# Kernel optimization log

Hardware: AMD Instinct MI355X
Metric: run time of the kernel (lower is better)

Reference implementation:

```python
import jax, jax.numpy as jnp
import numpy as np

N, L, E, H = 4, 2048, 1024, 16
D = E // H  # head_dim = 64


def setup_inputs() -> dict:
    key = jax.random.key(0)
    ks = jax.random.split(key, 9)
    return {
        "values": jax.random.normal(ks[0], (N, L, E), jnp.float32),
        "keys": jax.random.normal(ks[1], (N, L, E), jnp.float32),
        "queries": jax.random.normal(ks[2], (N, L, E), jnp.float32),
        "mask": jax.random.randint(ks[3], (N, 1, L, L), 0, 2, jnp.int32),
        "Wq": jax.random.normal(ks[4], (D, D), jnp.float32) * (1.0 / np.sqrt(D)),
        "Wk": jax.random.normal(ks[5], (D, D), jnp.float32) * (1.0 / np.sqrt(D)),
        "Wv": jax.random.normal(ks[6], (D, D), jnp.float32) * (1.0 / np.sqrt(D)),
        "Wo": jax.random.normal(ks[7], (E, E), jnp.float32) * (1.0 / np.sqrt(E)),
        "bo": jax.random.normal(ks[8], (E,), jnp.float32) * 0.01,
    }


def reference(values, keys, queries, mask, Wq, Wk, Wv, Wo, bo):
    n, ql, _ = queries.shape
    kl = keys.shape[1]
    # split heads: [N, L, H, D]
    q = queries.reshape(n, ql, H, D)
    k = keys.reshape(n, kl, H, D)
    v = values.reshape(n, kl, H, D)
    # per-head linear projections (torch Linear: x @ W.T), shared across heads
    q = jnp.einsum('nqhd,ed->nqhe', q, Wq)
    k = jnp.einsum('nkhd,ed->nkhe', k, Wk)
    v = jnp.einsum('nkhd,ed->nkhe', v, Wv)
    # scores [N, H, Q, K]
    energy = jnp.einsum('nqhd,nkhd->nhqk', q, k)
    energy = jnp.where(mask == 0, jnp.float32(-1e20), energy)
    attn = jax.nn.softmax(energy / jnp.sqrt(jnp.float32(E)), axis=3)
    out = jnp.einsum('nhqk,nkhd->nqhd', attn, v).reshape(n, ql, E)
    return out @ Wo.T + bo
```

## Files before the change

kernel.cpp:

```cpp
#include <hip/hip_runtime.h>
#include <stdint.h>


static constexpr int N_ = 4, L_ = 2048, E_ = 1024, H_ = 16, D_ = 64;

typedef __bf16 bf16_t;
typedef __attribute__((ext_vector_type(8))) __bf16 bf16x8;
typedef __attribute__((ext_vector_type(4))) float f32x4;
typedef __attribute__((ext_vector_type(16))) float f32x16;
typedef __attribute__((ext_vector_type(4))) unsigned int uint4v;
typedef __attribute__((ext_vector_type(2))) unsigned int uint2v;

__device__ __forceinline__ f32x16 mfma32(bf16x8 a, bf16x8 b, f32x16 c) {
    return __builtin_amdgcn_mfma_f32_32x32x16_bf16(a, b, c, 0, 0, 0);
}
__device__ __forceinline__ unsigned int pk2(float a, float b) {
    union { bf16_t h[2]; unsigned int u; } z;
    z.h[0] = (bf16_t)a; z.h[1] = (bf16_t)b;
    return z.u;
}
#define GLOAD16(g, l)                                                        \
    __builtin_amdgcn_global_load_lds(                                        \
        (const __attribute__((address_space(1))) void*)(g),                  \
        (__attribute__((address_space(3))) void*)(l), 16, 0, 0)

__global__ __launch_bounds__(256) void pack_mask_k(
    const int* __restrict__ mask, unsigned int* __restrict__ mpkT) {
    int wid  = blockIdx.x * 4 + (threadIdx.x >> 6);
    int lane = threadIdx.x & 63;
    int c = wid & 31;
    int q = (wid >> 5) & (L_ - 1);
    int n = wid >> 16;
    int v = mask[((size_t)n * L_ + q) * L_ + c * 64 + lane];
    unsigned long long b = __ballot(v != 0);
    if (lane == 0) {
        mpkT[((size_t)n * 64 + 2 * c) * L_ + q]     = (unsigned int)b;
        mpkT[((size_t)n * 64 + 2 * c + 1) * L_ + q] = (unsigned int)(b >> 32);
    }
}

__global__ __launch_bounds__(256) void cvt_wo_k(
    const float* __restrict__ Wo, bf16_t* __restrict__ WoB) {
    int i = blockIdx.x * 256 + threadIdx.x;
    WoB[i] = (bf16_t)Wo[i];
}

__global__ __launch_bounds__(256) void proj_mfma_k(
    const float* __restrict__ qin, const float* __restrict__ kin,
    const float* __restrict__ vin,
    const float* __restrict__ Wq, const float* __restrict__ Wk,
    const float* __restrict__ Wv,
    bf16_t* __restrict__ qB, bf16_t* __restrict__ kB, bf16_t* __restrict__ vT) {
    int which = blockIdx.z;
    int h = blockIdx.y;
    const float* in = (which == 0) ? qin : (which == 1) ? kin : vin;
    const float* W  = (which == 0) ? Wq  : (which == 1) ? Wk  : Wv;
    int w = threadIdx.x >> 6, lane = threadIdx.x & 63;
    int lo5 = lane & 31, hi = lane >> 5;
    int rbase = blockIdx.x * 128 + w * 32;
    int n = rbase >> 11;
    int lloc = rbase & (L_ - 1);
    int nh = n * H_ + h;

    bf16x8 xf[4];
    const float* xrow = in + (size_t)(rbase + lo5) * E_ + h * 64 + hi * 8;
    #pragma unroll
    for (int c = 0; c < 4; ++c) {
        float4 f0 = *(const float4*)(xrow + c * 16);
        float4 f1 = *(const float4*)(xrow + c * 16 + 4);
        bf16x8 v;
        v[0] = (bf16_t)f0.x; v[1] = (bf16_t)f0.y; v[2] = (bf16_t)f0.z; v[3] = (bf16_t)f0.w;
        v[4] = (bf16_t)f1.x; v[5] = (bf16_t)f1.y; v[6] = (bf16_t)f1.z; v[7] = (bf16_t)f1.w;
        xf[c] = v;
    }
    bf16x8 wf[2][4];
    #pragma unroll
    for (int t2 = 0; t2 < 2; ++t2) {
        const float* wrow = W + (size_t)(t2 * 32 + lo5) * 64 + hi * 8;
        #pragma unroll
        for (int c = 0; c < 4; ++c) {
            float4 f0 = *(const float4*)(wrow + c * 16);
            float4 f1 = *(const float4*)(wrow + c * 16 + 4);
            bf16x8 v;
            v[0] = (bf16_t)f0.x; v[1] = (bf16_t)f0.y; v[2] = (bf16_t)f0.z; v[3] = (bf16_t)f0.w;
            v[4] = (bf16_t)f1.x; v[5] = (bf16_t)f1.y; v[6] = (bf16_t)f1.z; v[7] = (bf16_t)f1.w;
            wf[t2][c] = v;
        }
    }
    f32x16 acc0, acc1;
    #pragma unroll
    for (int r = 0; r < 16; ++r) { acc0[r] = 0.f; acc1[r] = 0.f; }

    if (which != 2) {
        #pragma unroll
        for (int c = 0; c < 4; ++c) {
            acc0 = mfma32(xf[c], wf[0][c], acc0);
            acc1 = mfma32(xf[c], wf[1][c], acc1);
        }
        const float osc = (which == 0) ? (0.03125f * 1.44269504f) : 1.0f;
        bf16_t* outp = ((which == 0) ? qB : kB) + ((size_t)nh * L_ + lloc) * 64;
        #pragma unroll
        for (int r = 0; r < 16; ++r) {
            int qr = (r & 3) + 8 * (r >> 2) + 4 * hi;
            outp[qr * 64 + lo5]      = (bf16_t)(acc0[r] * osc);
            outp[qr * 64 + 32 + lo5] = (bf16_t)(acc1[r] * osc);
        }
    } else {
        #pragma unroll
        for (int c = 0; c < 4; ++c) {
            acc0 = mfma32(wf[0][c], xf[c], acc0);
            acc1 = mfma32(wf[1][c], xf[c], acc1);
        }
        bf16_t* outp = vT + (size_t)nh * 64 * L_ + lloc;
        #pragma unroll
        for (int r = 0; r < 16; ++r) {
            int dr = (r & 3) + 8 * (r >> 2) + 4 * hi;
            outp[(size_t)dr * L_ + lo5]        = (bf16_t)acc0[r];
            outp[(size_t)(dr + 32) * L_ + lo5] = (bf16_t)acc1[r];
        }
    }
}

__global__ __launch_bounds__(512) void attn_lds_k(
    const bf16_t* __restrict__ qB, const bf16_t* __restrict__ kB,
    const bf16_t* __restrict__ vT, const unsigned int* __restrict__ mpkT,
    bf16_t* __restrict__ aoB) {
    __shared__ alignas(16) unsigned char smem[16384];
    int b = blockIdx.x;
    int xcd = b & 7, idx = b >> 3;
    int nh = xcd * 8 + (idx >> 3);
    int qt = idx & 7;
    int n = nh >> 4, h = nh & 15;
    int tid = threadIdx.x;
    int w = tid >> 6, lane = tid & 63;
    int lo5 = lane & 31, hi = lane >> 5;
    int q0 = qt * 256 + w * 32;

    const bf16_t* qb = qB + ((size_t)nh * L_ + q0) * D_;
    const bf16_t* kblk = kB + (size_t)nh * L_ * D_;
    const bf16_t* vblk = vT + (size_t)nh * D_ * L_;
    const unsigned int* mptr = mpkT + (size_t)n * 64 * L_ + q0 + lo5;

    unsigned char* my_lds_base = smem + (size_t)(tid >> 6) * 1024;
    size_t g_off;
    if (tid < 256) {
        int r = tid >> 3, c = tid & 7;
        g_off = (size_t)r * 64 + ((c ^ (r & 7)) * 8);
    } else {
        int v = tid - 256;
        int d = v >> 2, j = v & 3;
        g_off = (size_t)d * L_ + ((j ^ ((d >> 1) & 3)) * 8);
    }
    const size_t gstep = (tid < 256) ? (size_t)(32 * 64) : (size_t)32;
    const bf16_t* gnext = ((tid < 256) ? kblk : vblk) + g_off;

    bf16x8 qf[4];
    #pragma unroll
    for (int c = 0; c < 4; ++c)
        qf[c] = *(const bf16x8*)(qb + lo5 * D_ + c * 16 + hi * 8);

    f32x16 o0, o1;
    #pragma unroll
    for (int r = 0; r < 16; ++r) { o0[r] = 0.f; o1[r] = 0.f; }
    float lsum = 0.f;
    int vsw = (lo5 >> 1) & 3;

    f32x16 kZero;
    #pragma unroll
    for (int r = 0; r < 16; ++r) kZero[r] = 0.f;

    GLOAD16(gnext, my_lds_base);  gnext += gstep;
    unsigned int mw = *mptr; mptr += L_;

    #pragma unroll 1
    for (int t = 0; t < 64; ++t) {
        int cur = t & 1;
        unsigned int mw_n = *mptr; mptr += L_;
        if (t < 63) {
            GLOAD16(gnext, my_lds_base + (cur ^ 1) * 8192);
            gnext += gstep;
            asm volatile("s_waitcnt vmcnt(1)" ::: "memory");
        } else {
            asm volatile("s_waitcnt vmcnt(0)" ::: "memory");
        }
        __builtin_amdgcn_s_barrier();
        __builtin_amdgcn_sched_barrier(0);

        const bf16_t* Kb = (const bf16_t*)(smem + cur * 8192);
        const bf16_t* Vb = Kb + 2048;
        __builtin_amdgcn_s_setprio(1);
        bf16x8 kf0 = *(const bf16x8*)(Kb + lo5 * 64 + ((hi ^ (lo5 & 7)) << 3));
        f32x16 st = mfma32(kf0, qf[0], kZero);
        #pragma unroll
        for (int c = 1; c < 4; ++c) {
            bf16x8 kfc = *(const bf16x8*)(Kb + lo5 * 64 +
                                          ((((c << 1) | hi) ^ (lo5 & 7)) << 3));
            st = mfma32(kfc, qf[c], st);
        }
        __builtin_amdgcn_s_setprio(0);
        const bf16_t* vrow0 = Vb + lo5 * 32;
        const bf16_t* vrow1 = Vb + (lo5 + 32) * 32;
        bf16x8 v00 = *(const bf16x8*)(vrow0 + ((hi ^ vsw) << 3));
        bf16x8 v01 = *(const bf16x8*)(vrow0 + (((2 | hi) ^ vsw) << 3));
        bf16x8 v10 = *(const bf16x8*)(vrow1 + ((hi ^ vsw) << 3));
        bf16x8 v11 = *(const bf16x8*)(vrow1 + (((2 | hi) ^ vsw) << 3));
        float p[16];
        #pragma unroll
        for (int r = 0; r < 16; ++r) p[r] = exp2f(st[r]);
        unsigned int mws = hi ? (mw >> 4) : mw;
        #pragma unroll
        for (int r = 0; r < 16; ++r) {
            int kr = (r & 3) + 8 * (r >> 2);
            int mm = __builtin_amdgcn_sbfe(mws, kr, 1);
            p[r] = __uint_as_float(__float_as_uint(p[r]) & (unsigned int)mm);
        }
        float s0 = (p[0] + p[1]) + (p[2] + p[3]);
        float s1 = (p[4] + p[5]) + (p[6] + p[7]);
        float s2 = (p[8] + p[9]) + (p[10] + p[11]);
        float s3 = (p[12] + p[13]) + (p[14] + p[15]);
        lsum += (s0 + s1) + (s2 + s3);
        unsigned int w0 = pk2(p[0],  p[1]),  w1 = pk2(p[2],  p[3]);
        unsigned int w2 = pk2(p[4],  p[5]),  w3 = pk2(p[6],  p[7]);
        unsigned int w4 = pk2(p[8],  p[9]),  w5 = pk2(p[10], p[11]);
        unsigned int w6 = pk2(p[12], p[13]), w7 = pk2(p[14], p[15]);
        uint2v s02 = __builtin_amdgcn_permlane32_swap(w0, w2, false, false);
        uint2v s13 = __builtin_amdgcn_permlane32_swap(w1, w3, false, false);
        uint2v s46 = __builtin_amdgcn_permlane32_swap(w4, w6, false, false);
        uint2v s57 = __builtin_amdgcn_permlane32_swap(w5, w7, false, false);
        uint4v fa0, fa1;
        fa0.x = s02.x; fa0.y = s13.x; fa0.z = s02.y; fa0.w = s13.y;
        fa1.x = s46.x; fa1.y = s57.x; fa1.z = s46.y; fa1.w = s57.y;
        bf16x8 pa0 = __builtin_bit_cast(bf16x8, fa0);
        bf16x8 pa1 = __builtin_bit_cast(bf16x8, fa1);
        __builtin_amdgcn_s_setprio(1);
        o0 = mfma32(pa0, v00, o0);
        o1 = mfma32(pa0, v10, o1);
        o0 = mfma32(pa1, v01, o0);
        o1 = mfma32(pa1, v11, o1);
        __builtin_amdgcn_s_setprio(0);
        mw = mw_n;
        __builtin_amdgcn_s_barrier();
        __builtin_amdgcn_sched_barrier(0);
    }

    float lt = lsum + __shfl_xor(lsum, 32);
    #pragma unroll
    for (int r = 0; r < 16; ++r) {
        int qr = (r & 3) + 8 * (r >> 2) + 4 * hi;
        float inv = __builtin_amdgcn_rcpf(__shfl(lt, qr));
        bf16_t* orow = aoB + ((size_t)n * L_ + q0 + qr) * E_ + h * 64;
        orow[lo5]      = (bf16_t)(o0[r] * inv);
        orow[32 + lo5] = (bf16_t)(o1[r] * inv);
    }
}

__global__ __launch_bounds__(256) void out_gemm_lds_k(
    const bf16_t* __restrict__ A, const bf16_t* __restrict__ WoB,
    const float* __restrict__ bo, float* __restrict__ Y) {
    __shared__ alignas(16) unsigned char bsm[32768];
    int b = blockIdx.x;
    int ct = b & 7, rt = b >> 3;
    int tid = threadIdx.x;
    int w = tid >> 6, lane = tid & 63;
    int lo5 = lane & 31, hi = lane >> 5;
    int row0 = rt * 128, col0 = ct * 128;
    const bf16_t* arow = A + (size_t)(row0 + w * 32 + lo5) * E_ + hi * 8;

    f32x16 acc0, acc1, acc2, acc3;
    #pragma unroll
    for (int r = 0; r < 16; ++r) { acc0[r]=0.f; acc1[r]=0.f; acc2[r]=0.f; acc3[r]=0.f; }

    auto stageB = [&](int kc, int buf) {
        #pragma unroll
        for (int rr = 0; rr < 4; ++rr) {
            int g = tid + rr * 256;
            int nn = g >> 3, slot = g & 7;
            const bf16_t* src = WoB + (size_t)(col0 + nn) * E_ + kc * 64 +
                                ((slot ^ (nn & 7)) * 8);
            GLOAD16(src, bsm + (size_t)buf * 16384 + (size_t)(w * 64 + rr * 256) * 16);
        }
    };

    stageB(0, 0);
    #pragma unroll 1
    for (int kc = 0; kc < 16; ++kc) {
        int cur = kc & 1;
        if (kc < 15) stageB(kc + 1, cur ^ 1);
        if (kc < 15) { asm volatile("s_waitcnt vmcnt(4)" ::: "memory"); }
        else         { asm volatile("s_waitcnt vmcnt(0)" ::: "memory"); }
        __builtin_amdgcn_s_barrier();
        __builtin_amdgcn_sched_barrier(0);
        const bf16_t* Bl = (const bf16_t*)(bsm + (size_t)cur * 16384);
        #pragma unroll
        for (int c = 0; c < 4; ++c) {
            bf16x8 af = *(const bf16x8*)(arow + kc * 64 + c * 16);
            int slot = ((((c << 1) | hi) ^ (lo5 & 7)) << 3);
            bf16x8 b0 = *(const bf16x8*)(Bl + (0 * 32 + lo5) * 64 + slot);
            bf16x8 b1 = *(const bf16x8*)(Bl + (1 * 32 + lo5) * 64 + slot);
            bf16x8 b2 = *(const bf16x8*)(Bl + (2 * 32 + lo5) * 64 + slot);
            bf16x8 b3 = *(const bf16x8*)(Bl + (3 * 32 + lo5) * 64 + slot);
            __builtin_amdgcn_s_setprio(1);
            acc0 = mfma32(af, b0, acc0);
            acc1 = mfma32(af, b1, acc1);
            acc2 = mfma32(af, b2, acc2);
            acc3 = mfma32(af, b3, acc3);
            __builtin_amdgcn_s_setprio(0);
        }
        __builtin_amdgcn_s_barrier();
        __builtin_amdgcn_sched_barrier(0);
    }

    #define EPI(ACC, CG)                                                     \
    {                                                                        \
        float bias = bo[col0 + (CG) * 32 + lo5];                             \
        _Pragma("unroll")                                                    \
        for (int r = 0; r < 16; ++r) {                                       \
            int qr = (r & 3) + 8 * (r >> 2) + 4 * hi;                        \
            Y[(size_t)(row0 + w * 32 + qr) * E_ + col0 + (CG) * 32 + lo5] =  \
                ACC[r] + bias;                                               \
        }                                                                    \
    }
    EPI(acc0, 0) EPI(acc1, 1) EPI(acc2, 2) EPI(acc3, 3)
    #undef EPI
}

extern "C" void kernel_launch(void* const* d_in, const int* in_sizes, int n_in,
                              void* d_out, int out_size, void* d_ws, size_t ws_size,
                              hipStream_t stream) {
    const float* values  = (const float*)d_in[0];
    const float* keys    = (const float*)d_in[1];
    const float* queries = (const float*)d_in[2];
    const int*   mask    = (const int*)  d_in[3];
    const float* Wq      = (const float*)d_in[4];
    const float* Wk      = (const float*)d_in[5];
    const float* Wv      = (const float*)d_in[6];
    const float* Wo      = (const float*)d_in[7];
    const float* bo      = (const float*)d_in[8];
    float* Y = (float*)d_out;

    const size_t SZ = (size_t)N_ * H_ * L_ * D_;
    bf16_t* qB  = (bf16_t*)d_ws;
    bf16_t* kB  = qB + SZ;
    bf16_t* vT  = kB + SZ;
    bf16_t* aoB = vT + SZ;
    unsigned int* mpkT = (unsigned int*)(aoB + SZ);
    bf16_t* WoB = (bf16_t*)(mpkT + (size_t)N_ * 64 * L_);

    pack_mask_k<<<N_ * L_ * 32 / 4, 256, 0, stream>>>(mask, mpkT);
    cvt_wo_k<<<E_ * E_ / 256, 256, 0, stream>>>(Wo, WoB);
    proj_mfma_k<<<dim3(N_ * L_ / 128, H_, 3), 256, 0, stream>>>(
        queries, keys, values, Wq, Wk, Wv, qB, kB, vT);
    attn_lds_k<<<N_ * H_ * (L_ / 256), 512, 0, stream>>>(
        qB, kB, vT, mpkT, aoB);
    out_gemm_lds_k<<<(E_ / 128) * (N_ * L_ / 128), 256, 0, stream>>>(
        aoB, WoB, bo, Y);
}
```

Before: 240.7 us.

## Halve attention block size and unroll double-buffered K/V loop by two

The attention kernel now launches 256-thread blocks covering 128 queries instead of 512-thread blocks covering 256. Twice as many blocks are launched, and each thread loads both K and V tiles instead of splitting the loads across thread halves. The main loop is unrolled by two with fixed buffer pointers, LDS offsets are precomputed, and it uses the raw exp2 builtin and packed float2 sums. The goal is more blocks per CU, less address arithmetic and lighter barriers. The cost is that each block re-reads the full K/V stream, so global and L2 traffic for K/V doubles.

```diff
diff --git a/kernel.cpp b/kernel.cpp
--- a/kernel.cpp
+++ b/kernel.cpp
@@ -6,6 +6,7 @@
 
 typedef __bf16 bf16_t;
 typedef __attribute__((ext_vector_type(8))) __bf16 bf16x8;
+typedef __attribute__((ext_vector_type(2))) float f32x2;
 typedef __attribute__((ext_vector_type(4))) float f32x4;
 typedef __attribute__((ext_vector_type(16))) float f32x16;
 typedef __attribute__((ext_vector_type(4))) unsigned int uint4v;
@@ -121,104 +122,92 @@
     }
 }
 
-__global__ __launch_bounds__(512) void attn_lds_k(
+__global__ __launch_bounds__(256) void attn_lds_k(
     const bf16_t* __restrict__ qB, const bf16_t* __restrict__ kB,
     const bf16_t* __restrict__ vT, const unsigned int* __restrict__ mpkT,
     bf16_t* __restrict__ aoB) {
     __shared__ alignas(16) unsigned char smem[16384];
     int b = blockIdx.x;
     int xcd = b & 7, idx = b >> 3;
-    int nh = xcd * 8 + (idx >> 3);
-    int qt = idx & 7;
+    int nh = xcd * 8 + (idx >> 4);
+    int qt = idx & 15;
     int n = nh >> 4, h = nh & 15;
     int tid = threadIdx.x;
     int w = tid >> 6, lane = tid & 63;
     int lo5 = lane & 31, hi = lane >> 5;
-    int q0 = qt * 256 + w * 32;
+    int q0 = qt * 128 + w * 32;
 
     const bf16_t* qb = qB + ((size_t)nh * L_ + q0) * D_;
     const bf16_t* kblk = kB + (size_t)nh * L_ * D_;
     const bf16_t* vblk = vT + (size_t)nh * D_ * L_;
     const unsigned int* mptr = mpkT + (size_t)n * 64 * L_ + q0 + lo5;
 
-    unsigned char* my_lds_base = smem + (size_t)(tid >> 6) * 1024;
-    size_t g_off;
-    if (tid < 256) {
-        int r = tid >> 3, c = tid & 7;
-        g_off = (size_t)r * 64 + ((c ^ (r & 7)) * 8);
-    } else {
-        int v = tid - 256;
-        int d = v >> 2, j = v & 3;
-        g_off = (size_t)d * L_ + ((j ^ ((d >> 1) & 3)) * 8);
-    }
-    const size_t gstep = (tid < 256) ? (size_t)(32 * 64) : (size_t)32;
-    const bf16_t* gnext = ((tid < 256) ? kblk : vblk) + g_off;
+    int kr_ = tid >> 3, kc_ = tid & 7;
+    int vd_ = tid >> 2, vj_ = tid & 3;
+    const bf16_t* gK = kblk + kr_ * 64 + ((kc_ ^ (kr_ & 7)) * 8);
+    const bf16_t* gV = vblk + (size_t)vd_ * L_ + ((vj_ ^ ((vd_ >> 1) & 3)) * 8);
+    unsigned ldsK = (unsigned)(w * 1024);
+    unsigned ldsV = (unsigned)(4096 + w * 1024);
 
     bf16x8 qf[4];
     #pragma unroll
     for (int c = 0; c < 4; ++c)
         qf[c] = *(const bf16x8*)(qb + lo5 * D_ + c * 16 + hi * 8);
 
+    int koff0 = lo5 * 64 + (((0 | hi) ^ (lo5 & 7)) << 3);
+    int koff1 = lo5 * 64 + (((2 | hi) ^ (lo5 & 7)) << 3);
+    int koff2 = lo5 * 64 + (((4 | hi) ^ (lo5 & 7)) << 3);
+    int koff3 = lo5 * 64 + (((6 | hi) ^ (lo5 & 7)) << 3);
+    int vsw = (lo5 >> 1) & 3;
+    int voff0a = lo5 * 32 + ((hi ^ vsw) << 3);
+    int voff0b = lo5 * 32 + (((2 | hi) ^ vsw) << 3);
+    int voff1a = (lo5 + 32) * 32 + ((hi ^ vsw) << 3);
+    int voff1b = (lo5 + 32) * 32 + (((2 | hi) ^ vsw) << 3);
+    int shv = hi << 2;
+
     f32x16 o0, o1;
     #pragma unroll
     for (int r = 0; r < 16; ++r) { o0[r] = 0.f; o1[r] = 0.f; }
     float lsum = 0.f;
-    int vsw = (lo5 >> 1) & 3;
-
     f32x16 kZero;
     #pragma unroll
     for (int r = 0; r < 16; ++r) kZero[r] = 0.f;
 
-    GLOAD16(gnext, my_lds_base);  gnext += gstep;
-    unsigned int mw = *mptr; mptr += L_;
-
-    #pragma unroll 1
-    for (int t = 0; t < 64; ++t) {
-        int cur = t & 1;
-        unsigned int mw_n = *mptr; mptr += L_;
-        if (t < 63) {
-            GLOAD16(gnext, my_lds_base + (cur ^ 1) * 8192);
-            gnext += gstep;
-            asm volatile("s_waitcnt vmcnt(1)" ::: "memory");
-        } else {
-            asm volatile("s_waitcnt vmcnt(0)" ::: "memory");
-        }
-        __builtin_amdgcn_s_barrier();
-        __builtin_amdgcn_sched_barrier(0);
-
-        const bf16_t* Kb = (const bf16_t*)(smem + cur * 8192);
-        const bf16_t* Vb = Kb + 2048;
+    auto stage = [&](int buf) {
+        GLOAD16(gK, smem + buf * 8192 + ldsK);
+        GLOAD16(gV, smem + buf * 8192 + ldsV);
+        gK += 32 * 64;
+        gV += 32;
+    };
+
+    auto body = [&](const bf16_t* Kb, const bf16_t* Vb, unsigned int mw) {
         __builtin_amdgcn_s_setprio(1);
-        bf16x8 kf0 = *(const bf16x8*)(Kb + lo5 * 64 + ((hi ^ (lo5 & 7)) << 3));
-        f32x16 st = mfma32(kf0, qf[0], kZero);
-        #pragma unroll
-        for (int c = 1; c < 4; ++c) {
-            bf16x8 kfc = *(const bf16x8*)(Kb + lo5 * 64 +
-                                          ((((c << 1) | hi) ^ (lo5 & 7)) << 3));
-            st = mfma32(kfc, qf[c], st);
-        }
+        f32x16 st = mfma32(*(const bf16x8*)(Kb + koff0), qf[0], kZero);
+        st = mfma32(*(const bf16x8*)(Kb + koff1), qf[1], st);
+        st = mfma32(*(const bf16x8*)(Kb + koff2), qf[2], st);
+        st = mfma32(*(const bf16x8*)(Kb + koff3), qf[3], st);
         __builtin_amdgcn_s_setprio(0);
-        const bf16_t* vrow0 = Vb + lo5 * 32;
-        const bf16_t* vrow1 = Vb + (lo5 + 32) * 32;
-        bf16x8 v00 = *(const bf16x8*)(vrow0 + ((hi ^ vsw) << 3));
-        bf16x8 v01 = *(const bf16x8*)(vrow0 + (((2 | hi) ^ vsw) << 3));
-        bf16x8 v10 = *(const bf16x8*)(vrow1 + ((hi ^ vsw) << 3));
-        bf16x8 v11 = *(const bf16x8*)(vrow1 + (((2 | hi) ^ vsw) << 3));
+        bf16x8 v00 = *(const bf16x8*)(Vb + voff0a);
+        bf16x8 v01 = *(const bf16x8*)(Vb + voff0b);
+        bf16x8 v10 = *(const bf16x8*)(Vb + voff1a);
+        bf16x8 v11 = *(const bf16x8*)(Vb + voff1b);
         float p[16];
         #pragma unroll
-        for (int r = 0; r < 16; ++r) p[r] = exp2f(st[r]);
-        unsigned int mws = hi ? (mw >> 4) : mw;
+        for (int r = 0; r < 16; ++r) p[r] = __builtin_amdgcn_exp2f(st[r]);
+        unsigned int mws = mw >> shv;
         #pragma unroll
         for (int r = 0; r < 16; ++r) {
             int kr = (r & 3) + 8 * (r >> 2);
             int mm = __builtin_amdgcn_sbfe(mws, kr, 1);
             p[r] = __uint_as_float(__float_as_uint(p[r]) & (unsigned int)mm);
         }
-        float s0 = (p[0] + p[1]) + (p[2] + p[3]);
-        float s1 = (p[4] + p[5]) + (p[6] + p[7]);
-        float s2 = (p[8] + p[9]) + (p[10] + p[11]);
-        float s3 = (p[12] + p[13]) + (p[14] + p[15]);
-        lsum += (s0 + s1) + (s2 + s3);
+        f32x2 q01 = (f32x2){p[0], p[1]}  + (f32x2){p[2], p[3]};
+        f32x2 q23 = (f32x2){p[4], p[5]}  + (f32x2){p[6], p[7]};
+        f32x2 q45 = (f32x2){p[8], p[9]}  + (f32x2){p[10], p[11]};
+        f32x2 q67 = (f32x2){p[12], p[13]} + (f32x2){p[14], p[15]};
+        f32x2 qa = q01 + q23, qb2 = q45 + q67;
+        f32x2 qc = qa + qb2;
+        lsum += qc.x + qc.y;
         unsigned int w0 = pk2(p[0],  p[1]),  w1 = pk2(p[2],  p[3]);
         unsigned int w2 = pk2(p[4],  p[5]),  w3 = pk2(p[6],  p[7]);
         unsigned int w4 = pk2(p[8],  p[9]),  w5 = pk2(p[10], p[11]);
@@ -238,9 +227,44 @@
         o0 = mfma32(pa1, v01, o0);
         o1 = mfma32(pa1, v11, o1);
         __builtin_amdgcn_s_setprio(0);
-        mw = mw_n;
-        __builtin_amdgcn_s_barrier();
-        __builtin_amdgcn_sched_barrier(0);
+    };
+
+    const bf16_t* K0 = (const bf16_t*)(smem);
+    const bf16_t* V0 = K0 + 2048;
+    const bf16_t* K1 = (const bf16_t*)(smem + 8192);
+    const bf16_t* V1 = K1 + 2048;
+
+    stage(0);
+    unsigned int mw = *mptr; mptr += L_;
+
+    #pragma unroll 1
+    for (int tt = 0; tt < 32; ++tt) {
+        {
+            unsigned int mw_n = *mptr; mptr += L_;
+            stage(1);
+            asm volatile("s_waitcnt vmcnt(2)" ::: "memory");
+            __builtin_amdgcn_s_barrier();
+            __builtin_amdgcn_sched_barrier(0);
+            body(K0, V0, mw);
+            mw = mw_n;
+            __builtin_amdgcn_s_barrier();
+            __builtin_amdgcn_sched_barrier(0);
+        }
+        {
+            unsigned int mw_n = *mptr; mptr += L_;
+            if (tt < 31) {
+                stage(0);
+                asm volatile("s_waitcnt vmcnt(2)" ::: "memory");
+            } else {
+                asm volatile("s_waitcnt vmcnt(0)" ::: "memory");
+            }
+            __builtin_amdgcn_s_barrier();
+            __builtin_amdgcn_sched_barrier(0);
+            body(K1, V1, mw);
+            mw = mw_n;
+            __builtin_amdgcn_s_barrier();
+            __builtin_amdgcn_sched_barrier(0);
+        }
     }
 
     float lt = lsum + __shfl_xor(lsum, 32);
@@ -350,7 +374,7 @@
     cvt_wo_k<<<E_ * E_ / 256, 256, 0, stream>>>(Wo, WoB);
     proj_mfma_k<<<dim3(N_ * L_ / 128, H_, 3), 256, 0, stream>>>(
         queries, keys, values, Wq, Wk, Wv, qB, kB, vT);
-    attn_lds_k<<<N_ * H_ * (L_ / 256), 512, 0, stream>>>(
+    attn_lds_k<<<N_ * H_ * (L_ / 128), 256, 0, stream>>>(
         qB, kB, vT, mpkT, aoB);
     out_gemm_lds_k<<<(E_ / 128) * (N_ * L_ / 128), 256, 0, stream>>>(
         aoB, WoB, bo, Y);
```

Result: faster. 228.1 us (-5.2%).
